# Kernel optimization log

Hardware: AMD Instinct MI355X
Metric: run time of the kernel (lower is better)

## Reference

```python
import jax, jax.numpy as jnp
import numpy as np

NUM_HEADS = 12
HEAD_DIM = 64
EPS = 1e-5


def _ln(t, g, b):
    m = t.mean(-1, keepdims=True)
    v = ((t - m) ** 2).mean(-1, keepdims=True)
    return (t - m) * jax.lax.rsqrt(v + EPS) * g + b


def _pool(t, conv_w, g, b, B, H, W, C):
    # t: [B, heads, 1+H*W, C] -> depthwise-conv pooled [B, heads, 1+Hp*Wp, C]
    cls = t[:, :, :1, :]
    sp = t[:, :, 1:, :].reshape(B * NUM_HEADS, H, W, C).transpose(0, 3, 1, 2)
    y = jax.lax.conv_general_dilated(
        sp, conv_w, (2, 2), [(1, 1), (1, 1)],
        feature_group_count=C,
        dimension_numbers=('NCHW', 'OIHW', 'NCHW'))
    Hp, Wp = y.shape[2], y.shape[3]
    y = y.reshape(B, NUM_HEADS, C, Hp * Wp).transpose(0, 1, 3, 2)
    y = jnp.concatenate([cls, y], axis=2)
    return _ln(y, g, b), (Hp, Wp)


def _rel_dist(q_s, k_s):
    q_ratio = max(k_s / q_s, 1.0)
    k_ratio = max(q_s / k_s, 1.0)
    d = jnp.arange(q_s)[:, None] * q_ratio - jnp.arange(k_s)[None, :] * k_ratio
    d = d + (k_s - 1) * k_ratio
    return d.astype(jnp.int32)


def _forward(x, pool_q_w, pool_k_w, pool_v_w,
             norm_q_g, norm_q_b, norm_k_g, norm_k_b, norm_v_g, norm_v_b,
             wq, bq, wk, bk, wv, bv, proj_w, proj_b,
             rel_pos_h, rel_pos_w, feat_h, feat_w):
    B, N, D = x.shape
    C = D // NUM_HEADS
    t = x.reshape(B, N, NUM_HEADS, C).transpose(0, 2, 1, 3)  # [B,h,N,C]
    q, (qh, qw) = _pool(t, pool_q_w, norm_q_g, norm_q_b, B, feat_h, feat_w, C)
    k, (kh, kw) = _pool(t, pool_k_w, norm_k_g, norm_k_b, B, feat_h, feat_w, C)
    v, _ = _pool(t, pool_v_w, norm_v_g, norm_v_b, B, feat_h, feat_w, C)

    def proj_heads(y, w, bias):
        n = y.shape[2]
        y = y.transpose(0, 2, 1, 3).reshape(B, n, D)
        y = y @ w + bias
        return y.reshape(B, n, NUM_HEADS, HEAD_DIM).transpose(0, 2, 1, 3)

    q = proj_heads(q, wq, bq)
    k = proj_heads(k, wk, bk)
    v = proj_heads(v, wv, bv)

    scale = HEAD_DIM ** -0.5
    attn = jnp.einsum('bhqd,bhkd->bhqk', q * scale, k)

    # spatial relative position bias (cal_rel_pos_type), cls token excluded
    Rh = rel_pos_h[_rel_dist(qh, kh)]   # [qh,kh,hd]
    Rw = rel_pos_w[_rel_dist(qw, kw)]   # [qw,kw,hd]
    r_q = q[:, :, 1:, :].reshape(B, NUM_HEADS, qh, qw, HEAD_DIM)
    rel_h = jnp.einsum('byhwc,hkc->byhwk', r_q, Rh)
    rel_w = jnp.einsum('byhwc,wkc->byhwk', r_q, Rw)
    bias2d = (rel_h[..., :, None] + rel_w[..., None, :]).reshape(
        B, NUM_HEADS, qh * qw, kh * kw)
    attn = attn.at[:, :, 1:, 1:].add(bias2d)

    attn = jax.nn.softmax(attn, axis=-1)
    out = jnp.einsum('bhqk,bhkd->bhqd', attn, v)
    out = out + q  # residual pooling
    out = out.transpose(0, 2, 1, 3).reshape(B, -1, NUM_HEADS * HEAD_DIM)
    return out @ proj_w + proj_b


def setup_inputs() -> dict:
    key = jax.random.key(0)
    ks = jax.random.split(key, 16)
    B, D, C = 16, 768, 64
    H = W = 56
    N = H * W + 1
    rs = 2 * 28 - 1
    rnd = lambda i, sh, s: jax.random.normal(ks[i], sh, jnp.float32) * s
    return {
        'x': rnd(0, (B, N, D), 1.0),
        'pool_q_w': rnd(1, (C, 1, 3, 3), 0.1),
        'pool_k_w': rnd(2, (C, 1, 3, 3), 0.1),
        'pool_v_w': rnd(3, (C, 1, 3, 3), 0.1),
        'norm_q_g': jnp.ones((C,), jnp.float32),
        'norm_q_b': jnp.zeros((C,), jnp.float32),
        'norm_k_g': jnp.ones((C,), jnp.float32),
        'norm_k_b': jnp.zeros((C,), jnp.float32),
        'norm_v_g': jnp.ones((C,), jnp.float32),
        'norm_v_b': jnp.zeros((C,), jnp.float32),
        'wq': rnd(4, (D, D), 0.02), 'bq': jnp.zeros((D,), jnp.float32),
        'wk': rnd(5, (D, D), 0.02), 'bk': jnp.zeros((D,), jnp.float32),
        'wv': rnd(6, (D, D), 0.02), 'bv': jnp.zeros((D,), jnp.float32),
        'proj_w': rnd(7, (D, D), 0.02), 'proj_b': jnp.zeros((D,), jnp.float32),
        'rel_pos_h': rnd(8, (rs, HEAD_DIM), 0.02),
        'rel_pos_w': rnd(9, (rs, HEAD_DIM), 0.02),
        'feat_h': 56, 'feat_w': 56,
    }


def reference(x, pool_q_w, pool_k_w, pool_v_w,
              norm_q_g, norm_q_b, norm_k_g, norm_k_b, norm_v_g, norm_v_b,
              wq, bq, wk, bk, wv, bv, proj_w, proj_b,
              rel_pos_h, rel_pos_w, feat_h, feat_w):
    return _forward(x, pool_q_w, pool_k_w, pool_v_w,
                    norm_q_g, norm_q_b, norm_k_g, norm_k_b,
                    norm_v_g, norm_v_b,
                    wq, bq, wk, bk, wv, bv, proj_w, proj_b,
                    rel_pos_h, rel_pos_w, int(feat_h), int(feat_w))
```

## Files before the change

kernel.cpp:

```cpp
#include <hip/hip_runtime.h>
#include <stdint.h>

#define NUM_HEADS 12
#define HEAD_DIM  64
#define HWDIM     56
#define PHDIM     28
#define NTOK      785
#define NIN       3137
#define BATCH     16
#define DMODEL    768
#define BHCNT     192
#define LOG2E     1.44269504f

typedef __attribute__((ext_vector_type(8))) short bf16x8;
typedef __attribute__((ext_vector_type(4))) short s16x4;
typedef __attribute__((ext_vector_type(4))) float f32x4;

static __device__ __forceinline__ float bf2f(short s) {
  unsigned u = ((unsigned)(unsigned short)s) << 16;
  float f; __builtin_memcpy(&f, &u, 4); return f;
}
static __device__ __forceinline__ short f2bf(float f) {
  unsigned u; __builtin_memcpy(&u, &f, 4);
  unsigned r = u + 0x7FFFu + ((u >> 16) & 1u);
  return (short)(r >> 16);
}
static __device__ __forceinline__ float fexp2(float x) {
#if defined(__has_builtin)
#if __has_builtin(__builtin_amdgcn_exp2f)
  return __builtin_amdgcn_exp2f(x);
#else
  return exp2f(x);
#endif
#else
  return exp2f(x);
#endif
}

static __device__ __forceinline__ int xcd_chunk(int orig, int nwg) {
  int xcd = orig & 7;
  int within = orig >> 3;
  int q = nwg >> 3, r = nwg & 7;
  int base = (xcd < r) ? xcd * (q + 1) : r * (q + 1) + (xcd - r) * q;
  return base + within;
}

#if defined(__has_builtin)
#if __has_builtin(__builtin_amdgcn_global_load_lds)
#define HAVE_GLLDS 1
#endif
#endif

static __device__ __forceinline__ void gl_lds16(const short* g, short* l) {
#ifdef HAVE_GLLDS
  __builtin_amdgcn_global_load_lds(
      (const __attribute__((address_space(1))) void*)g,
      (__attribute__((address_space(3))) void*)l, 16, 0, 0);
#else
  int lane = threadIdx.x & 63;
  *(bf16x8*)(l + lane * 8) = *(const bf16x8*)g;
#endif
}

__global__ __launch_bounds__(192) void pool_ln_kernel(
    const float* __restrict__ x,
    const float* __restrict__ wq9, const float* __restrict__ wk9, const float* __restrict__ wv9,
    const float* __restrict__ gq, const float* __restrict__ bq,
    const float* __restrict__ gk, const float* __restrict__ bk,
    const float* __restrict__ gv, const float* __restrict__ bv,
    short* __restrict__ Pq, short* __restrict__ Pk, short* __restrict__ Pv)
{
  __shared__ __align__(16) float wt_s[3][9][64];
  int tid = threadIdx.x;
  int blk = xcd_chunk(blockIdx.x, 16 * 197);
  int b = blk / 197;
  int n0 = (blk - b * 197) * 4;

  for (int idx = tid; idx < 3 * 576; idx += 192) {
    int conv = idx / 576, rem = idx - conv * 576;
    int c = rem / 9, tap = rem - c * 9;
    const float* wsrc = (conv == 0) ? wq9 : (conv == 1) ? wk9 : wv9;
    wt_s[conv][tap][c] = wsrc[c * 9 + tap];
  }
  __syncthreads();

  int ch0 = tid * 4;
  int c4 = ch0 & 63;
  f32x4 g_q = *(const f32x4*)&gq[c4], b_q = *(const f32x4*)&bq[c4];
  f32x4 g_k = *(const f32x4*)&gk[c4], b_k = *(const f32x4*)&bk[c4];
  f32x4 g_v = *(const f32x4*)&gv[c4], b_v = *(const f32x4*)&bv[c4];

  for (int tt = 0; tt < 4; ++tt) {
    int n = n0 + tt;
    if (n >= NTOK) break;
    f32x4 aq = (f32x4){0.f, 0.f, 0.f, 0.f}, ak = aq, av = aq;
    if (n == 0) {
      f32x4 x4 = *(const f32x4*)&x[((size_t)b * NIN) * DMODEL + ch0];
      aq = ak = av = x4;
    } else {
      int s = n - 1;
      int i = s / PHDIM, j = s - i * PHDIM;
#pragma unroll
      for (int di = 0; di < 3; ++di) {
        int ii = 2 * i - 1 + di;
        if (ii < 0 || ii >= HWDIM) continue;
#pragma unroll
        for (int dj = 0; dj < 3; ++dj) {
          int jj = 2 * j - 1 + dj;
          if (jj < 0 || jj >= HWDIM) continue;
          f32x4 x4 = *(const f32x4*)&x[((size_t)b * NIN + 1 + ii * HWDIM + jj) * DMODEL + ch0];
          int tap = di * 3 + dj;
          f32x4 w0 = *(const f32x4*)&wt_s[0][tap][c4];
          f32x4 w1 = *(const f32x4*)&wt_s[1][tap][c4];
          f32x4 w2 = *(const f32x4*)&wt_s[2][tap][c4];
          aq += w0 * x4; ak += w1 * x4; av += w2 * x4;
        }
      }
    }
    size_t obase = ((size_t)b * NTOK + n) * DMODEL + ch0;
    {
      float sm = aq[0] + aq[1] + aq[2] + aq[3];
#pragma unroll
      for (int m = 1; m < 16; m <<= 1) sm += __shfl_xor(sm, m);
      float mn = sm * (1.f / 64.f);
      f32x4 d = aq - mn;
      float vs = d[0]*d[0] + d[1]*d[1] + d[2]*d[2] + d[3]*d[3];
#pragma unroll
      for (int m = 1; m < 16; m <<= 1) vs += __shfl_xor(vs, m);
      float rs = rsqrtf(vs * (1.f / 64.f) + 1e-5f);
      s16x4 o;
#pragma unroll
      for (int e = 0; e < 4; ++e) o[e] = f2bf(d[e] * rs * g_q[e] + b_q[e]);
      *(s16x4*)&Pq[obase] = o;
    }
    {
      float sm = ak[0] + ak[1] + ak[2] + ak[3];
#pragma unroll
      for (int m = 1; m < 16; m <<= 1) sm += __shfl_xor(sm, m);
      float mn = sm * (1.f / 64.f);
      f32x4 d = ak - mn;
      float vs = d[0]*d[0] + d[1]*d[1] + d[2]*d[2] + d[3]*d[3];
#pragma unroll
      for (int m = 1; m < 16; m <<= 1) vs += __shfl_xor(vs, m);
      float rs = rsqrtf(vs * (1.f / 64.f) + 1e-5f);
      s16x4 o;
#pragma unroll
      for (int e = 0; e < 4; ++e) o[e] = f2bf(d[e] * rs * g_k[e] + b_k[e]);
      *(s16x4*)&Pk[obase] = o;
    }
    {
      float sm = av[0] + av[1] + av[2] + av[3];
#pragma unroll
      for (int m = 1; m < 16; m <<= 1) sm += __shfl_xor(sm, m);
      float mn = sm * (1.f / 64.f);
      f32x4 d = av - mn;
      float vs = d[0]*d[0] + d[1]*d[1] + d[2]*d[2] + d[3]*d[3];
#pragma unroll
      for (int m = 1; m < 16; m <<= 1) vs += __shfl_xor(vs, m);
      float rs = rsqrtf(vs * (1.f / 64.f) + 1e-5f);
      s16x4 o;
#pragma unroll
      for (int e = 0; e < 4; ++e) o[e] = f2bf(d[e] * rs * g_v[e] + b_v[e]);
      *(s16x4*)&Pv[obase] = o;
    }
  }
}

__global__ __launch_bounds__(256) void trans_kernel(
    const float* __restrict__ s0, const float* __restrict__ s1,
    const float* __restrict__ s2, const float* __restrict__ s3,
    short* __restrict__ d0, short* __restrict__ d1,
    short* __restrict__ d2, short* __restrict__ d3)
{
  __shared__ float tile[32][33];
  int z = blockIdx.z;
  const float* s = (z == 0) ? s0 : (z == 1) ? s1 : (z == 2) ? s2 : s3;
  short* d = (z == 0) ? d0 : (z == 1) ? d1 : (z == 2) ? d2 : d3;
  int k0 = blockIdx.x * 32, n0 = blockIdx.y * 32;
  int tx = threadIdx.x, ty = threadIdx.y;
#pragma unroll
  for (int jj = 0; jj < 4; ++jj)
    tile[ty + jj * 8][tx] = s[(size_t)(k0 + ty + jj * 8) * DMODEL + n0 + tx];
  __syncthreads();
#pragma unroll
  for (int jj = 0; jj < 4; ++jj)
    d[(size_t)(n0 + ty + jj * 8) * DMODEL + k0 + tx] = f2bf(tile[tx][ty + jj * 8]);
}

static __device__ __forceinline__ void gemm_core(
    short* As, short* Bs,
    const short* __restrict__ A, const short* __restrict__ Bt,
    const float* __restrict__ bias, void* __restrict__ outp, void* __restrict__ outp2,
    int rowbase, int colbase, int M, int Nn, int mode)
{
  const int K = DMODEL;
  int tid = threadIdx.x;
  int wid = tid >> 6, lane = tid & 63;
  int lg = lane >> 4, lq = lane & 15;
  int wm = wid >> 1, wn = wid & 1;

  f32x4 acc[4][4];
#pragma unroll
  for (int i = 0; i < 4; ++i)
#pragma unroll
    for (int j = 0; j < 4; ++j) acc[i][j] = (f32x4){0.f, 0.f, 0.f, 0.f};

  int srow = tid >> 2;
  int scol = (tid & 3) * 8;
  int ar0 = min(rowbase + srow, M - 1);
  int ar1 = min(rowbase + 64 + srow, M - 1);
  int br0 = min(colbase + srow, Nn - 1);
  int br1 = min(colbase + 64 + srow, Nn - 1);
  const short* Ag0 = A + (size_t)ar0 * K + scol;
  const short* Ag1 = A + (size_t)ar1 * K + scol;
  const short* Bg0 = Bt + (size_t)br0 * K + scol;
  const short* Bg1 = Bt + (size_t)br1 * K + scol;

  auto stage = [&](int kt, int buf) __attribute__((always_inline)) {
    short* Ab = As + buf * 4096;
    short* Bb = Bs + buf * 4096;
    gl_lds16(Ag0 + kt, Ab + wid * 512);
    gl_lds16(Ag1 + kt, Ab + 2048 + wid * 512);
    gl_lds16(Bg0 + kt, Bb + wid * 512);
    gl_lds16(Bg1 + kt, Bb + 2048 + wid * 512);
  };

  stage(0, 0);
  __syncthreads();
  int cur = 0;
  for (int kt = 0; kt < K; kt += 32) {
    if (kt + 32 < K) stage(kt + 32, cur ^ 1);
    const short* Ac = As + cur * 4096;
    const short* Bc = Bs + cur * 4096;
    bf16x8 aFrag[4], bFrag[4];
#pragma unroll
    for (int mi = 0; mi < 4; ++mi)
      aFrag[mi] = *(const bf16x8*)&Ac[(wm * 64 + mi * 16 + lq) * 32 + lg * 8];
#pragma unroll
    for (int ni = 0; ni < 4; ++ni)
      bFrag[ni] = *(const bf16x8*)&Bc[(wn * 64 + ni * 16 + lq) * 32 + lg * 8];
    __builtin_amdgcn_s_setprio(1);
#pragma unroll
    for (int mi = 0; mi < 4; ++mi)
#pragma unroll
      for (int ni = 0; ni < 4; ++ni)
        acc[mi][ni] = __builtin_amdgcn_mfma_f32_16x16x32_bf16(aFrag[mi], bFrag[ni], acc[mi][ni], 0, 0, 0);
    __builtin_amdgcn_s_setprio(0);
    __syncthreads();
    cur ^= 1;
  }

  if (mode >= 3) {
    const float s2 = 0.125f * LOG2E;
    int myhead = (colbase >> 6) + wn;
#pragma unroll
    for (int mi = 0; mi < 4; ++mi) {
      int rowq = rowbase + wm * 64 + mi * 16 + lg * 4;
#pragma unroll
      for (int r = 0; r < 4; ++r) {
        int row = rowq + r;
        if (row < M) {
          int bb = row / NTOK, nn = row - bb * NTOK;
          size_t abase = ((size_t)(bb * NUM_HEADS + myhead) * NTOK + nn) * 128;
#pragma unroll
          for (int ni = 0; ni < 4; ++ni) {
            int col = colbase + wn * 64 + ni * 16 + lq;
            int c = col & 63;
            float v = acc[mi][ni][r] + bias[col];
            if (mode == 3) {
              ((short*)outp)[(((size_t)(bb * NUM_HEADS + myhead) * NTOK + nn) << 6) + c] = f2bf(v);
              ((short*)outp2)[abase + c] = f2bf(v * s2);
            } else {
              ((short*)outp2)[abase + c] = f2bf(v);
            }
          }
        }
      }
    }
    int rz = rowbase + wm * 64 + lane;
    if (rz < M) {
      int bb = rz / NTOK, nn = rz - bb * NTOK;
      short* dst = (short*)outp2 + ((size_t)(bb * NUM_HEADS + myhead) * NTOK + nn) * 128 + 64;
      if (mode == 3) {
        bf16x8 z = {0, 0, 0, 0, 0, 0, 0, 0};
#pragma unroll
        for (int zc = 0; zc < 8; ++zc) *(bf16x8*)(dst + zc * 8) = z;
      } else {
        int ki = -100, kj = -100;
        if (nn >= 1) { int km1 = nn - 1; ki = km1 / PHDIM; kj = km1 - ki * PHDIM; }
#pragma unroll
        for (int zc = 0; zc < 8; ++zc) {
          bf16x8 o = {0, 0, 0, 0, 0, 0, 0, 0};
#pragma unroll
          for (int e = 0; e < 8; ++e) {
            int d = 64 + zc * 8 + e;
            if (d == 64 + ki || d == 92 + kj) o[e] = (short)0x3F80;
          }
          *(bf16x8*)(dst + zc * 8) = o;
        }
      }
    }
    return;
  }

#pragma unroll
  for (int mi = 0; mi < 4; ++mi) {
    int rowq = rowbase + wm * 64 + mi * 16 + lg * 4;
#pragma unroll
    for (int r = 0; r < 4; ++r) {
      int row = rowq + r;
      if (row < M) {
        if (mode == 2) {
          float bb = bias[row];
#pragma unroll
          for (int ni = 0; ni < 4; ++ni) {
            int col = colbase + wn * 64 + ni * 16 + lq;
            if (col < Nn) {
              int b = col / NTOK, n = col - b * NTOK;
              float v = acc[mi][ni][r] + bb;
              ((short*)outp)[((size_t)b * DMODEL + row) * NTOK + n] = f2bf(v);
            }
          }
        } else {
          int bb = row / NTOK;
          int nn = row - bb * NTOK;
#pragma unroll
          for (int ni = 0; ni < 4; ++ni) {
            int col = colbase + wn * 64 + ni * 16 + lq;
            float v = acc[mi][ni][r] + bias[col];
            if (mode == 0) {
              ((float*)outp)[(size_t)row * DMODEL + col] = v;
            } else {
              ((short*)outp)[(((size_t)(bb * NUM_HEADS + (col >> 6)) * NTOK + nn) << 6) + (col & 63)] = f2bf(v);
            }
          }
        }
      }
    }
  }
}

__global__ __launch_bounds__(256) void gemm_qkv_kernel(
    const short* __restrict__ Pq, const short* __restrict__ WqT,
    const float* __restrict__ bq, short* __restrict__ qhd, short* __restrict__ qaug,
    const short* __restrict__ Pk, const short* __restrict__ WkT,
    const float* __restrict__ bk, short* __restrict__ kaug,
    const short* __restrict__ WvT, const short* __restrict__ Pv,
    const float* __restrict__ bv, short* __restrict__ vtg)
{
  __shared__ short As[2 * 4096];
  __shared__ short Bs[2 * 4096];
  const int NWG = 1782;
  int lid = xcd_chunk(blockIdx.x, NWG);
  if (lid < 1188) {
    int which = lid / 594;
    int sub = lid - which * 594;
    int rowbase = (sub / 6) * 128;
    int colbase = (sub % 6) * 128;
    if (which == 0)
      gemm_core(As, Bs, Pq, WqT, bq, (void*)qhd, (void*)qaug,
                rowbase, colbase, BATCH * NTOK, DMODEL, 3);
    else
      gemm_core(As, Bs, Pk, WkT, bk, nullptr, (void*)kaug,
                rowbase, colbase, BATCH * NTOK, DMODEL, 4);
  } else {
    int sub = lid - 1188;
    int rowbase = (sub % 6) * 128;
    int colbase = (sub / 6) * 128;
    gemm_core(As, Bs, WvT, Pv, bv, (void*)vtg, nullptr,
              rowbase, colbase, DMODEL, BATCH * NTOK, 2);
  }
}

__global__ __launch_bounds__(256) void gemm_proj_kernel(
    const short* __restrict__ Afin, const short* __restrict__ WpT,
    const float* __restrict__ bp, float* __restrict__ outp)
{
  __shared__ short As[2 * 4096];
  __shared__ short Bs[2 * 4096];
  const int NWG = 594;
  int lid = xcd_chunk(blockIdx.x, NWG);
  int rowbase = (lid / 6) * 128;
  int colbase = (lid % 6) * 128;
  gemm_core(As, Bs, Afin, WpT, bp, (void*)outp, nullptr,
            rowbase, colbase, BATCH * NTOK, DMODEL, 0);
}

__global__ __launch_bounds__(256) void relbias_kernel(
    const short* __restrict__ qh, const float* __restrict__ rph,
    const float* __restrict__ rpw, short* __restrict__ qaug)
{
  int line = blockIdx.x;
  int bh = blockIdx.y;
  int mode = blockIdx.z;
  __shared__ __align__(16) float qt_s[28 * 68];
  __shared__ __align__(16) float rt_s[28 * 68];
  int tid = threadIdx.x;
  const float* rp = (mode == 0) ? rph : rpw;
  for (int idx = tid; idx < 28 * 64; idx += 256) {
    int rr = idx >> 6, c = idx & 63;
    int qi = (mode == 0) ? (1 + line * PHDIM + rr) : (1 + rr * PHDIM + line);
    qt_s[rr * 68 + c] = bf2f(qh[((size_t)bh * NTOK + qi) * HEAD_DIM + c]);
    rt_s[rr * 68 + c] = rp[(line - rr + 27) * HEAD_DIM + c];
  }
  __syncthreads();
  for (int o = tid; o < 784; o += 256) {
    int kk = o / PHDIM, rr = o - kk * PHDIM;
    const f32x4* qa = (const f32x4*)&qt_s[rr * 68];
    const f32x4* ra = (const f32x4*)&rt_s[kk * 68];
    f32x4 a4 = (f32x4){0.f, 0.f, 0.f, 0.f};
#pragma unroll
    for (int i = 0; i < 16; ++i) a4 += qa[i] * ra[i];
    float s = (a4[0] + a4[1] + a4[2] + a4[3]) * LOG2E;
    int qi = (mode == 0) ? (1 + line * PHDIM + rr) : (1 + rr * PHDIM + line);
    int dim = (mode == 0) ? (64 + kk) : (92 + kk);
    qaug[((size_t)bh * NTOK + qi) * 128 + dim] = f2bf(s);
  }
}

__global__ __launch_bounds__(256) void flash7_kernel(
    const short* __restrict__ qaug, const short* __restrict__ qh,
    const short* __restrict__ kaug, const short* __restrict__ vtg,
    short* __restrict__ Afin)
{
  int id = blockIdx.x;
  int slot = id >> 3;
  int bh = (id & 7) * 24 + slot / 13;
  int qt = slot - (slot / 13) * 13;
  int qbase = qt * 64;
  int tid = threadIdx.x, wid = tid >> 6, lane = tid & 63;
  int lg = lane >> 4, lq = lane & 15;

  __shared__ __align__(16) short ks[64 * 128];
  __shared__ __align__(16) short vt[64 * 64];
  __shared__ __align__(16) float axl[4][16];

  int qi0 = qbase + wid * 16 + lq;
  int qiq = min(qi0, NTOK - 1);
  const short* qrow = qaug + ((size_t)bh * NTOK + qiq) * 128;
  bf16x8 bq[4];
#pragma unroll
  for (int c = 0; c < 4; ++c) bq[c] = *(const bf16x8*)(qrow + c * 32 + lg * 8);

  float m_l = -3e30f, l_l = 0.f;
  f32x4 acc[4];
#pragma unroll
  for (int ch = 0; ch < 4; ++ch) acc[ch] = (f32x4){0.f, 0.f, 0.f, 0.f};

  const short* kbase = kaug + (size_t)bh * NTOK * 128;
  const short* vbase = vtg + (size_t)bh * (size_t)HEAD_DIM * NTOK;

  int koffK[4], kslot[4];
#pragma unroll
  for (int m = 0; m < 4; ++m) {
    int c = m * 256 + tid;
    int rr = c >> 4, j = c & 15;
    koffK[m] = ((rr & 15) >> 2) * 16 + (rr >> 4) * 4 + (rr & 3);
    kslot[m] = (j ^ (rr & 15)) << 3;
  }
  int c0 = tid, c1 = 256 + tid;
  int vr0 = c0 >> 3, vj0 = c0 & 7;
  int vr1 = c1 >> 3, vj1 = c1 & 7;
  const short* vsrc0 = vbase + (size_t)vr0 * NTOK + ((vj0 ^ (vr0 & 7)) << 3);
  const short* vsrc1 = vbase + (size_t)vr1 * NTOK + ((vj1 ^ (vr1 & 7)) << 3);

  auto step_body = [&](int kvb, bool last) __attribute__((always_inline)) {
    __syncthreads();
#pragma unroll
    for (int m = 0; m < 4; ++m)
      gl_lds16(kbase + (size_t)min(kvb + koffK[m], NTOK - 1) * 128 + kslot[m],
               ks + m * 2048 + wid * 512);
    gl_lds16(vsrc0 + kvb, vt + wid * 512);
    gl_lds16(vsrc1 + kvb, vt + 2048 + wid * 512);
    __syncthreads();

    float p[16];
#pragma unroll
    for (int kt = 0; kt < 4; ++kt) {
      int kl = kt * 16 + lq;
      const char* kp = (const char*)ks + kl * 256;
      int swz = kl & 15;
      f32x4 s = (f32x4){0.f, 0.f, 0.f, 0.f};
      __builtin_amdgcn_s_setprio(1);
#pragma unroll
      for (int c = 0; c < 4; ++c) {
        bf16x8 aK = *(const bf16x8*)(kp + (((c * 4 + lg) ^ swz) << 4));
        s = __builtin_amdgcn_mfma_f32_16x16x32_bf16(aK, bq[c], s, 0, 0, 0);
      }
      __builtin_amdgcn_s_setprio(0);
#pragma unroll
      for (int r = 0; r < 4; ++r) {
        int i = kt * 4 + r;
        float v = s[r];
        if (last) {
          int key = kvb + 16 * lg + i;
          if (key >= NTOK) v = -3e30f;
        }
        p[i] = v;
      }
    }

    float pm = p[0];
#pragma unroll
    for (int i = 1; i < 16; ++i) pm = fmaxf(pm, p[i]);
    pm = fmaxf(pm, __shfl_xor(pm, 16));
    pm = fmaxf(pm, __shfl_xor(pm, 32));
    if (!__all(pm - m_l <= 11.5f)) {
      float mnew = fmaxf(m_l, pm);
      float alpha = fexp2(m_l - mnew);
      m_l = mnew;
      l_l *= alpha;
      if (lg == 0) axl[wid][lq] = alpha;
      f32x4 av = *(const f32x4*)&axl[wid][lg * 4];
#pragma unroll
      for (int ch = 0; ch < 4; ++ch)
#pragma unroll
        for (int r = 0; r < 4; ++r) acc[ch][r] *= av[r];
    }
    float ps = 0.f;
#pragma unroll
    for (int i = 0; i < 16; ++i) { p[i] = fexp2(p[i] - m_l); ps += p[i]; }
    ps += __shfl_xor(ps, 16);
    ps += __shfl_xor(ps, 32);
    l_l += ps;

    bf16x8 pa0, pa1;
#pragma unroll
    for (int j = 0; j < 4; ++j) {
      unsigned u0, u1, v0, v1;
      __builtin_memcpy(&u0, &p[2 * j], 4);
      __builtin_memcpy(&u1, &p[2 * j + 1], 4);
      __builtin_memcpy(&v0, &p[8 + 2 * j], 4);
      __builtin_memcpy(&v1, &p[8 + 2 * j + 1], 4);
      ((unsigned*)&pa0)[j] = (u0 >> 16) | (u1 & 0xFFFF0000u);
      ((unsigned*)&pa1)[j] = (v0 >> 16) | (v1 & 0xFFFF0000u);
    }
    __builtin_amdgcn_s_setprio(1);
#pragma unroll
    for (int ch = 0; ch < 4; ++ch) {
      int d = ch * 16 + lq;
      const char* vrow = (const char*)vt + d * 128;
      int swz = lq & 7;
      bf16x8 bv0 = *(const bf16x8*)(vrow + (((2 * lg + 0) ^ swz) << 4));
      bf16x8 bv1 = *(const bf16x8*)(vrow + (((2 * lg + 1) ^ swz) << 4));
      acc[ch] = __builtin_amdgcn_mfma_f32_16x16x32_bf16(pa0, bv0, acc[ch], 0, 0, 0);
      acc[ch] = __builtin_amdgcn_mfma_f32_16x16x32_bf16(pa1, bv1, acc[ch], 0, 0, 0);
    }
    __builtin_amdgcn_s_setprio(0);
  };

  for (int step = 0; step < 12; ++step) step_body(step * 64, false);
  step_body(12 * 64, true);

  if (lg == 0) axl[wid][lq] = l_l;
  f32x4 lv = *(const f32x4*)&axl[wid][lg * 4];
  int b = bh / NUM_HEADS, h = bh - b * NUM_HEADS;
#pragma unroll
  for (int r = 0; r < 4; ++r) {
    int qi = qbase + wid * 16 + lg * 4 + r;
    if (qi < NTOK) {
      float inv = 1.f / lv[r];
#pragma unroll
      for (int ch = 0; ch < 4; ++ch) {
        int d = ch * 16 + lq;
        float o = acc[ch][r] * inv + bf2f(qh[((size_t)bh * NTOK + qi) * HEAD_DIM + d]);
        Afin[((size_t)b * NTOK + qi) * DMODEL + h * HEAD_DIM + d] = f2bf(o);
      }
    }
  }
}

extern "C" void kernel_launch(void* const* d_in, const int* in_sizes, int n_in,
                              void* d_out, int out_size, void* d_ws, size_t ws_size,
                              hipStream_t stream)
{
  (void)in_sizes; (void)n_in; (void)out_size; (void)ws_size;
  const float* x   = (const float*)d_in[0];
  const float* pqw = (const float*)d_in[1];
  const float* pkw = (const float*)d_in[2];
  const float* pvw = (const float*)d_in[3];
  const float* gq  = (const float*)d_in[4];
  const float* bq_ = (const float*)d_in[5];
  const float* gk  = (const float*)d_in[6];
  const float* bk_ = (const float*)d_in[7];
  const float* gv  = (const float*)d_in[8];
  const float* bv_ = (const float*)d_in[9];
  const float* wq  = (const float*)d_in[10];
  const float* bqp = (const float*)d_in[11];
  const float* wk  = (const float*)d_in[12];
  const float* bkp = (const float*)d_in[13];
  const float* wv  = (const float*)d_in[14];
  const float* bvp = (const float*)d_in[15];
  const float* wp  = (const float*)d_in[16];
  const float* bpp = (const float*)d_in[17];
  const float* rph = (const float*)d_in[18];
  const float* rpw = (const float*)d_in[19];

  char* ws = (char*)d_ws;
  size_t off = 0;
  auto alloc = [&](size_t bytes) -> void* {
    void* p = ws + off; off += (bytes + 255) & ~(size_t)255; return p;
  };
  const size_t MROWS = (size_t)BATCH * NTOK;
  short* Pq  = (short*)alloc(MROWS * DMODEL * 2);
  short* Pk  = (short*)alloc(MROWS * DMODEL * 2);
  short* Pv  = (short*)alloc(MROWS * DMODEL * 2);
  short* WqT = (short*)alloc((size_t)DMODEL * DMODEL * 2);
  short* WkT = (short*)alloc((size_t)DMODEL * DMODEL * 2);
  short* WvT = (short*)alloc((size_t)DMODEL * DMODEL * 2);
  short* WpT = (short*)alloc((size_t)DMODEL * DMODEL * 2);
  short* qhd = (short*)alloc(MROWS * DMODEL * 2 + 4096);
  short* vtg = (short*)alloc(MROWS * DMODEL * 2 + 8192);
  short* qaug = (short*)alloc((size_t)BHCNT * NTOK * 128 * 2 + 8192);
  short* kaug = (short*)alloc((size_t)BHCNT * NTOK * 128 * 2 + 8192);
  short* Afin = (short*)alloc(MROWS * DMODEL * 2);

  pool_ln_kernel<<<dim3(16 * 197), 192, 0, stream>>>(
      x, pqw, pkw, pvw, gq, bq_, gk, bk_, gv, bv_, Pq, Pk, Pv);
  trans_kernel<<<dim3(24, 24, 4), dim3(32, 8), 0, stream>>>(
      wq, wk, wv, wp, WqT, WkT, WvT, WpT);
  gemm_qkv_kernel<<<dim3(1782), 256, 0, stream>>>(
      Pq, WqT, bqp, qhd, qaug, Pk, WkT, bkp, kaug, WvT, Pv, bvp, vtg);
  relbias_kernel<<<dim3(28, BHCNT, 2), 256, 0, stream>>>(qhd, rph, rpw, qaug);
  flash7_kernel<<<dim3(2496), 256, 0, stream>>>(qaug, qhd, kaug, vtg, Afin);
  gemm_proj_kernel<<<dim3(594), 256, 0, stream>>>(Afin, WpT, bpp, (float*)d_out);
}
```

Measured before the change: 355.5 us.

## Use BK=64 XOR-swizzled LDS tiles in GEMM and drop separate q buffer

The shared GEMM core now stages 64-wide K tiles with an XOR swizzle on the LDS layout, which halves the number of barriers per K loop and aims to avoid LDS bank conflicts. LDS use doubles to 64 KB per block, which may lower occupancy. Separately, the q projection no longer writes a second unscaled q copy; qaug stores unscaled q, and the softmax scale is applied to the scores inside the flash kernel. The relative-bias values are pre-multiplied by 8 so they come out right after that scaling, and the residual now reads q from qaug.

New measurement: 397.1 us. 11.7% more time.

```diff
diff --git a/kernel.cpp b/kernel.cpp
--- a/kernel.cpp
+++ b/kernel.cpp
@@ -205,53 +205,64 @@
 #pragma unroll
     for (int j = 0; j < 4; ++j) acc[i][j] = (f32x4){0.f, 0.f, 0.f, 0.f};
 
-  int srow = tid >> 2;
-  int scol = (tid & 3) * 8;
-  int ar0 = min(rowbase + srow, M - 1);
-  int ar1 = min(rowbase + 64 + srow, M - 1);
-  int br0 = min(colbase + srow, Nn - 1);
-  int br1 = min(colbase + 64 + srow, Nn - 1);
-  const short* Ag0 = A + (size_t)ar0 * K + scol;
-  const short* Ag1 = A + (size_t)ar1 * K + scol;
-  const short* Bg0 = Bt + (size_t)br0 * K + scol;
-  const short* Bg1 = Bt + (size_t)br1 * K + scol;
+  const short* AgP[4];
+  const short* BgP[4];
+#pragma unroll
+  for (int m = 0; m < 4; ++m) {
+    int ch = m * 256 + tid;
+    int row = ch >> 3, j = ch & 7;
+    int gcol = (j ^ (row & 7)) << 3;
+    int ar = min(rowbase + row, M - 1);
+    int br = min(colbase + row, Nn - 1);
+    AgP[m] = A + (size_t)ar * K + gcol;
+    BgP[m] = Bt + (size_t)br * K + gcol;
+  }
 
   auto stage = [&](int kt, int buf) __attribute__((always_inline)) {
-    short* Ab = As + buf * 4096;
-    short* Bb = Bs + buf * 4096;
-    gl_lds16(Ag0 + kt, Ab + wid * 512);
-    gl_lds16(Ag1 + kt, Ab + 2048 + wid * 512);
-    gl_lds16(Bg0 + kt, Bb + wid * 512);
-    gl_lds16(Bg1 + kt, Bb + 2048 + wid * 512);
+    short* Ab = As + buf * 8192;
+    short* Bb = Bs + buf * 8192;
+#pragma unroll
+    for (int m = 0; m < 4; ++m) {
+      gl_lds16(AgP[m] + kt, Ab + m * 2048 + wid * 512);
+      gl_lds16(BgP[m] + kt, Bb + m * 2048 + wid * 512);
+    }
   };
 
   stage(0, 0);
   __syncthreads();
   int cur = 0;
-  for (int kt = 0; kt < K; kt += 32) {
-    if (kt + 32 < K) stage(kt + 32, cur ^ 1);
-    const short* Ac = As + cur * 4096;
-    const short* Bc = Bs + cur * 4096;
-    bf16x8 aFrag[4], bFrag[4];
-#pragma unroll
-    for (int mi = 0; mi < 4; ++mi)
-      aFrag[mi] = *(const bf16x8*)&Ac[(wm * 64 + mi * 16 + lq) * 32 + lg * 8];
-#pragma unroll
-    for (int ni = 0; ni < 4; ++ni)
-      bFrag[ni] = *(const bf16x8*)&Bc[(wn * 64 + ni * 16 + lq) * 32 + lg * 8];
-    __builtin_amdgcn_s_setprio(1);
-#pragma unroll
-    for (int mi = 0; mi < 4; ++mi)
-#pragma unroll
-      for (int ni = 0; ni < 4; ++ni)
-        acc[mi][ni] = __builtin_amdgcn_mfma_f32_16x16x32_bf16(aFrag[mi], bFrag[ni], acc[mi][ni], 0, 0, 0);
-    __builtin_amdgcn_s_setprio(0);
+  for (int kt = 0; kt < K; kt += 64) {
+    if (kt + 64 < K) stage(kt + 64, cur ^ 1);
+    const short* Ac = As + cur * 8192;
+    const short* Bc = Bs + cur * 8192;
+#pragma unroll
+    for (int kk = 0; kk < 2; ++kk) {
+      bf16x8 aFrag[4], bFrag[4];
+#pragma unroll
+      for (int mi = 0; mi < 4; ++mi) {
+        int r = wm * 64 + mi * 16 + lq;
+        int slot = (kk * 4 + lg) ^ (r & 7);
+        aFrag[mi] = *(const bf16x8*)&Ac[r * 64 + slot * 8];
+      }
+#pragma unroll
+      for (int ni = 0; ni < 4; ++ni) {
+        int r = wn * 64 + ni * 16 + lq;
+        int slot = (kk * 4 + lg) ^ (r & 7);
+        bFrag[ni] = *(const bf16x8*)&Bc[r * 64 + slot * 8];
+      }
+      __builtin_amdgcn_s_setprio(1);
+#pragma unroll
+      for (int mi = 0; mi < 4; ++mi)
+#pragma unroll
+        for (int ni = 0; ni < 4; ++ni)
+          acc[mi][ni] = __builtin_amdgcn_mfma_f32_16x16x32_bf16(aFrag[mi], bFrag[ni], acc[mi][ni], 0, 0, 0);
+      __builtin_amdgcn_s_setprio(0);
+    }
     __syncthreads();
     cur ^= 1;
   }
 
   if (mode >= 3) {
-    const float s2 = 0.125f * LOG2E;
     int myhead = (colbase >> 6) + wn;
 #pragma unroll
     for (int mi = 0; mi < 4; ++mi) {
@@ -267,12 +278,7 @@
             int col = colbase + wn * 64 + ni * 16 + lq;
             int c = col & 63;
             float v = acc[mi][ni][r] + bias[col];
-            if (mode == 3) {
-              ((short*)outp)[(((size_t)(bb * NUM_HEADS + myhead) * NTOK + nn) << 6) + c] = f2bf(v);
-              ((short*)outp2)[abase + c] = f2bf(v * s2);
-            } else {
-              ((short*)outp2)[abase + c] = f2bf(v);
-            }
+            ((short*)outp2)[abase + c] = f2bf(v);
           }
         }
       }
@@ -322,17 +328,11 @@
             }
           }
         } else {
-          int bb = row / NTOK;
-          int nn = row - bb * NTOK;
 #pragma unroll
           for (int ni = 0; ni < 4; ++ni) {
             int col = colbase + wn * 64 + ni * 16 + lq;
             float v = acc[mi][ni][r] + bias[col];
-            if (mode == 0) {
-              ((float*)outp)[(size_t)row * DMODEL + col] = v;
-            } else {
-              ((short*)outp)[(((size_t)(bb * NUM_HEADS + (col >> 6)) * NTOK + nn) << 6) + (col & 63)] = f2bf(v);
-            }
+            ((float*)outp)[(size_t)row * DMODEL + col] = v;
           }
         }
       }
@@ -342,14 +342,14 @@
 
 __global__ __launch_bounds__(256) void gemm_qkv_kernel(
     const short* __restrict__ Pq, const short* __restrict__ WqT,
-    const float* __restrict__ bq, short* __restrict__ qhd, short* __restrict__ qaug,
+    const float* __restrict__ bq, short* __restrict__ qaug,
     const short* __restrict__ Pk, const short* __restrict__ WkT,
     const float* __restrict__ bk, short* __restrict__ kaug,
     const short* __restrict__ WvT, const short* __restrict__ Pv,
     const float* __restrict__ bv, short* __restrict__ vtg)
 {
-  __shared__ short As[2 * 4096];
-  __shared__ short Bs[2 * 4096];
+  __shared__ short As[2 * 8192];
+  __shared__ short Bs[2 * 8192];
   const int NWG = 1782;
   int lid = xcd_chunk(blockIdx.x, NWG);
   if (lid < 1188) {
@@ -358,7 +358,7 @@
     int rowbase = (sub / 6) * 128;
     int colbase = (sub % 6) * 128;
     if (which == 0)
-      gemm_core(As, Bs, Pq, WqT, bq, (void*)qhd, (void*)qaug,
+      gemm_core(As, Bs, Pq, WqT, bq, nullptr, (void*)qaug,
                 rowbase, colbase, BATCH * NTOK, DMODEL, 3);
     else
       gemm_core(As, Bs, Pk, WkT, bk, nullptr, (void*)kaug,
@@ -376,8 +376,8 @@
     const short* __restrict__ Afin, const short* __restrict__ WpT,
     const float* __restrict__ bp, float* __restrict__ outp)
 {
-  __shared__ short As[2 * 4096];
-  __shared__ short Bs[2 * 4096];
+  __shared__ short As[2 * 8192];
+  __shared__ short Bs[2 * 8192];
   const int NWG = 594;
   int lid = xcd_chunk(blockIdx.x, NWG);
   int rowbase = (lid / 6) * 128;
@@ -387,7 +387,7 @@
 }
 
 __global__ __launch_bounds__(256) void relbias_kernel(
-    const short* __restrict__ qh, const float* __restrict__ rph,
+    const short* __restrict__ qaug_in, const float* __restrict__ rph,
     const float* __restrict__ rpw, short* __restrict__ qaug)
 {
   int line = blockIdx.x;
@@ -400,7 +400,7 @@
   for (int idx = tid; idx < 28 * 64; idx += 256) {
     int rr = idx >> 6, c = idx & 63;
     int qi = (mode == 0) ? (1 + line * PHDIM + rr) : (1 + rr * PHDIM + line);
-    qt_s[rr * 68 + c] = bf2f(qh[((size_t)bh * NTOK + qi) * HEAD_DIM + c]);
+    qt_s[rr * 68 + c] = bf2f(qaug_in[((size_t)bh * NTOK + qi) * 128 + c]);
     rt_s[rr * 68 + c] = rp[(line - rr + 27) * HEAD_DIM + c];
   }
   __syncthreads();
@@ -411,7 +411,7 @@
     f32x4 a4 = (f32x4){0.f, 0.f, 0.f, 0.f};
 #pragma unroll
     for (int i = 0; i < 16; ++i) a4 += qa[i] * ra[i];
-    float s = (a4[0] + a4[1] + a4[2] + a4[3]) * LOG2E;
+    float s = (a4[0] + a4[1] + a4[2] + a4[3]) * 8.0f;
     int qi = (mode == 0) ? (1 + line * PHDIM + rr) : (1 + rr * PHDIM + line);
     int dim = (mode == 0) ? (64 + kk) : (92 + kk);
     qaug[((size_t)bh * NTOK + qi) * 128 + dim] = f2bf(s);
@@ -419,9 +419,8 @@
 }
 
 __global__ __launch_bounds__(256) void flash7_kernel(
-    const short* __restrict__ qaug, const short* __restrict__ qh,
-    const short* __restrict__ kaug, const short* __restrict__ vtg,
-    short* __restrict__ Afin)
+    const short* __restrict__ qaug, const short* __restrict__ kaug,
+    const short* __restrict__ vtg, short* __restrict__ Afin)
 {
   int id = blockIdx.x;
   int slot = id >> 3;
@@ -447,6 +446,7 @@
 #pragma unroll
   for (int ch = 0; ch < 4; ++ch) acc[ch] = (f32x4){0.f, 0.f, 0.f, 0.f};
 
+  const float s2 = 0.125f * LOG2E;
   const short* kbase = kaug + (size_t)bh * NTOK * 128;
   const short* vbase = vtg + (size_t)bh * (size_t)HEAD_DIM * NTOK;
 
@@ -491,7 +491,7 @@
 #pragma unroll
       for (int r = 0; r < 4; ++r) {
         int i = kt * 4 + r;
-        float v = s[r];
+        float v = s[r] * s2;
         if (last) {
           int key = kvb + 16 * lg + i;
           if (key >= NTOK) v = -3e30f;
@@ -563,7 +563,7 @@
 #pragma unroll
       for (int ch = 0; ch < 4; ++ch) {
         int d = ch * 16 + lq;
-        float o = acc[ch][r] * inv + bf2f(qh[((size_t)bh * NTOK + qi) * HEAD_DIM + d]);
+        float o = acc[ch][r] * inv + bf2f(qaug[((size_t)bh * NTOK + qi) * 128 + d]);
         Afin[((size_t)b * NTOK + qi) * DMODEL + h * HEAD_DIM + d] = f2bf(o);
       }
     }
@@ -609,7 +609,6 @@
   short* WkT = (short*)alloc((size_t)DMODEL * DMODEL * 2);
   short* WvT = (short*)alloc((size_t)DMODEL * DMODEL * 2);
   short* WpT = (short*)alloc((size_t)DMODEL * DMODEL * 2);
-  short* qhd = (short*)alloc(MROWS * DMODEL * 2 + 4096);
   short* vtg = (short*)alloc(MROWS * DMODEL * 2 + 8192);
   short* qaug = (short*)alloc((size_t)BHCNT * NTOK * 128 * 2 + 8192);
   short* kaug = (short*)alloc((size_t)BHCNT * NTOK * 128 * 2 + 8192);
@@ -620,8 +619,8 @@
   trans_kernel<<<dim3(24, 24, 4), dim3(32, 8), 0, stream>>>(
       wq, wk, wv, wp, WqT, WkT, WvT, WpT);
   gemm_qkv_kernel<<<dim3(1782), 256, 0, stream>>>(
-      Pq, WqT, bqp, qhd, qaug, Pk, WkT, bkp, kaug, WvT, Pv, bvp, vtg);
-  relbias_kernel<<<dim3(28, BHCNT, 2), 256, 0, stream>>>(qhd, rph, rpw, qaug);
-  flash7_kernel<<<dim3(2496), 256, 0, stream>>>(qaug, qhd, kaug, vtg, Afin);
+      Pq, WqT, bqp, qaug, Pk, WkT, bkp, kaug, WvT, Pv, bvp, vtg);
+  relbias_kernel<<<dim3(28, BHCNT, 2), 256, 0, stream>>>(qaug, rph, rpw, qaug);
+  flash7_kernel<<<dim3(2496), 256, 0, stream>>>(qaug, kaug, vtg, Afin);
   gemm_proj_kernel<<<dim3(594), 256, 0, stream>>>(Afin, WpT, bpp, (float*)d_out);
 }
```
